# Optimization experiments

Hardware: AMD Instinct MI355X
Metric: run time of the kernel (lower is better)

## Reference

```python
import jax, jax.numpy as jnp
import numpy as np

N_HEAD = 16

def setup_inputs() -> dict:
    key = jax.random.key(0)
    ks = jax.random.split(key, 5)
    B, T, C = 4, 2048, 1024
    x = jax.random.normal(ks[0], (B, T, C), dtype=jnp.float32)
    # Linear params (torch nn.Linear: y = x @ W.T + b), init scaled like default
    s = 1.0 / np.sqrt(C)
    W_attn = jax.random.uniform(ks[1], (3 * C, C), dtype=jnp.float32, minval=-s, maxval=s)
    b_attn = jax.random.uniform(ks[2], (3 * C,), dtype=jnp.float32, minval=-s, maxval=s)
    W_proj = jax.random.uniform(ks[3], (C, C), dtype=jnp.float32, minval=-s, maxval=s)
    b_proj = jax.random.uniform(ks[4], (C,), dtype=jnp.float32, minval=-s, maxval=s)
    return {"x": x, "W_attn": W_attn, "b_attn": b_attn, "W_proj": W_proj, "b_proj": b_proj}

def reference(x, W_attn, b_attn, W_proj, b_proj):
    B, T, C = x.shape
    H = N_HEAD
    D = C // H
    qkv = jnp.einsum('btc,oc->bto', x, W_attn) + b_attn  # [B,T,3C]
    q, k, v = jnp.split(qkv, 3, axis=2)
    # [B,H,T,D]
    q = q.reshape(B, T, H, D).transpose(0, 2, 1, 3)
    k = k.reshape(B, T, H, D).transpose(0, 2, 1, 3)
    v = v.reshape(B, T, H, D).transpose(0, 2, 1, 3)
    att = jnp.einsum('bhtd,bhsd->bhts', q, k) * (1.0 / np.sqrt(D))  # [B,H,T,T]
    causal = jnp.tril(jnp.ones((T, T), dtype=bool))
    att = jnp.where(causal, att, -jnp.inf)
    att = jax.nn.softmax(att, axis=-1)
    y = jnp.einsum('bhts,bhsd->bhtd', att, v)  # [B,H,T,D]
    y = y.transpose(0, 2, 1, 3).reshape(B, T, C)
    return jnp.einsum('btc,oc->bto', y, W_proj) + b_proj
```

## Files before the change

### kernel.cpp

```cpp
#include <hip/hip_runtime.h>
#include <stdint.h>

typedef unsigned short u16;
typedef __attribute__((ext_vector_type(8))) short short8;
typedef __attribute__((ext_vector_type(4))) float float4v;

#define MFMA16(a, b, c) __builtin_amdgcn_mfma_f32_16x16x32_bf16((a), (b), (c), 0, 0, 0)

#define Q_SCALE 0.18033688011112042f

__device__ __forceinline__ int swz(int row, int col) {
  return row * 64 + (col & 7) + ((((col >> 3) ^ row) & 7) << 3);
}

__device__ __forceinline__ u16 f2b(float f) {
  union { float f; unsigned u; } x; x.f = f;
  unsigned r = x.u + 0x7fffu + ((x.u >> 16) & 1u);
  return (u16)(r >> 16);
}

__device__ __forceinline__ unsigned pack2(float a, float b) {
  return (unsigned)f2b(a) | ((unsigned)f2b(b) << 16);
}

__device__ __forceinline__ void load_lds_16(const void* g, void* l) {
  __builtin_amdgcn_global_load_lds((__attribute__((address_space(1))) void*)g,
                                   (__attribute__((address_space(3))) void*)l,
                                   16, 0, 0);
}

__global__ __launch_bounds__(256) void cvt_bf16(const float* __restrict__ in,
                                                u16* __restrict__ out, int n8) {
  int i = blockIdx.x * 256 + threadIdx.x;
  if (i >= n8) return;
  const float4* p = (const float4*)in + (size_t)i * 2;
  float4 a = p[0], b = p[1];
  uint4 w;
  w.x = pack2(a.x, a.y);
  w.y = pack2(a.z, a.w);
  w.z = pack2(b.x, b.y);
  w.w = pack2(b.z, b.w);
  *(uint4*)&out[(size_t)i * 8] = w;
}

__global__ __launch_bounds__(256) void transpose_v(const u16* __restrict__ V,
                                                   u16* __restrict__ Vt) {
  __shared__ u16 tile[64][72];
  const int bh = blockIdx.y;
  const int t0 = blockIdx.x * 64;
  const int tid = threadIdx.x;
  const int r = tid >> 3, c = (tid & 7) * 8;
#pragma unroll
  for (int h = 0; h < 2; ++h) {
    uint4 v = *(const uint4*)&V[((size_t)bh * 2048 + t0 + r + h * 32) * 64 + c];
    const u16* p = (const u16*)&v;
#pragma unroll
    for (int j = 0; j < 8; ++j) tile[c + j][r + h * 32] = p[j];
  }
  __syncthreads();
#pragma unroll
  for (int h = 0; h < 2; ++h) {
    uint4 w;
    u16* p = (u16*)&w;
#pragma unroll
    for (int j = 0; j < 8; ++j) p[j] = tile[r + h * 32][c + j];
    *(uint4*)&Vt[((size_t)bh * 64 + r + h * 32) * 2048 + t0 + c] = w;
  }
}

template <bool QKV_OUT>
__global__ __launch_bounds__(256) void gemm_bt(const u16* __restrict__ A,
                                               const u16* __restrict__ B,
                                               const float* __restrict__ bias,
                                               float* __restrict__ Cf,
                                               u16* __restrict__ QKV,
                                               int M, int N, int K) {
  __shared__ __align__(16) u16 As[128 * 64];
  __shared__ __align__(16) u16 Bs[128 * 64];
  const int tid = threadIdx.x;
  const int lane = tid & 63;
  const int wave = tid >> 6;
  const int quad = lane >> 4;
  const int l15 = lane & 15;
  const int bm0 = blockIdx.y * 128;
  const int bn0 = blockIdx.x * 128;
  const int wm = (wave & 1) * 64;
  const int wn = (wave >> 1) * 64;

  float4v acc[4][4];
#pragma unroll
  for (int i = 0; i < 4; ++i)
#pragma unroll
    for (int j = 0; j < 4; ++j) acc[i][j] = (float4v){0.f, 0.f, 0.f, 0.f};

  const int srow = wave * 32 + (lane >> 3);
  const int scol = ((lane & 7) ^ ((lane >> 3) & 7)) * 8;

  for (int k0 = 0; k0 < K; k0 += 64) {
#pragma unroll
    for (int s = 0; s < 4; ++s) {
      const int r = s * 8;
      load_lds_16(&A[(size_t)(bm0 + srow + r) * K + k0 + scol], &As[(wave * 32 + r) * 64]);
      load_lds_16(&B[(size_t)(bn0 + srow + r) * K + k0 + scol], &Bs[(wave * 32 + r) * 64]);
    }
    __builtin_amdgcn_s_waitcnt(0);
    __syncthreads();
#pragma unroll
    for (int ks = 0; ks < 2; ++ks) {
      short8 af[4], bf[4];
#pragma unroll
      for (int t = 0; t < 4; ++t) {
        af[t] = *(const short8*)&As[swz(wm + t * 16 + l15, ks * 32 + quad * 8)];
        bf[t] = *(const short8*)&Bs[swz(wn + t * 16 + l15, ks * 32 + quad * 8)];
      }
#pragma unroll
      for (int mt = 0; mt < 4; ++mt)
#pragma unroll
        for (int nt = 0; nt < 4; ++nt)
          acc[mt][nt] = MFMA16(af[mt], bf[nt], acc[mt][nt]);
    }
    __syncthreads();
  }

#pragma unroll
  for (int mt = 0; mt < 4; ++mt) {
    const int row0 = bm0 + wm + mt * 16 + quad * 4;
#pragma unroll
    for (int nt = 0; nt < 4; ++nt) {
      const int col = bn0 + wn + nt * 16 + l15;
      const float bs = bias[col];
      if constexpr (QKV_OUT) {
        const int which = col >> 10;
        const int rem = col & 1023;
        const int h = rem >> 6;
        const int d = rem & 63;
        const float sc = (which == 0) ? Q_SCALE : 1.0f;
#pragma unroll
        for (int i = 0; i < 4; ++i) {
          const int t = row0 + i;
          const int b = t >> 11;
          const int tt = t & 2047;
          QKV[(size_t)which * 8388608 +
              ((size_t)(b * 16 + h) * 2048 + tt) * 64 + d] = f2b((acc[mt][nt][i] + bs) * sc);
        }
      } else {
#pragma unroll
        for (int i = 0; i < 4; ++i)
          Cf[(size_t)(row0 + i) * N + col] = acc[mt][nt][i] + bs;
      }
    }
  }
}

__global__ __launch_bounds__(256) void attn_kernel(const u16* __restrict__ QKV,
                                                   const u16* __restrict__ Vt_g,
                                                   u16* __restrict__ Y) {
  const int bx = blockIdx.x;
  const int bh = blockIdx.y;
  const int b = bh >> 4, h = bh & 15;
  const int tid = threadIdx.x;
  const int lane = tid & 63;
  const int wave = tid >> 6;
  const int quad = lane >> 4;
  const int l15 = lane & 15;
  const int qt[2] = {bx, 31 - bx};

  const u16* Qg = QKV + (size_t)bh * 2048 * 64;
  const u16* Kg = QKV + 8388608 + (size_t)bh * 2048 * 64;
  const u16* Vg = Vt_g + (size_t)bh * 64 * 2048;

  __shared__ __align__(16) u16 Ks[2][64 * 64];
  __shared__ __align__(16) u16 Vt[2][64 * 64];

  short8 qf[2][2];
#pragma unroll
  for (int u = 0; u < 2; ++u)
#pragma unroll
    for (int ks = 0; ks < 2; ++ks)
      qf[u][ks] = *(const short8*)&Qg[(size_t)(qt[u] * 64 + wave * 16 + l15) * 64 + ks * 32 + quad * 8];

  float4v o[2][4];
  float rs[2] = {0.f, 0.f};
#pragma unroll
  for (int u = 0; u < 2; ++u)
#pragma unroll
    for (int i = 0; i < 4; ++i) o[u][i] = (float4v){0.f, 0.f, 0.f, 0.f};

  const int idxA = (l15 + ((quad & 1) << 5)) << 2;
  const int idxB = idxA + 64;

  const int r8 = lane >> 3;
  const int c8 = ((lane & 7) ^ r8) * 8;
  auto stage = [&](int st_, int bufi) {
    const int sb = st_ * 64;
#pragma unroll
    for (int p = 0; p < 2; ++p) {
      const int c = wave * 2 + p;
      load_lds_16(&Kg[(size_t)(sb + c * 8 + r8) * 64 + c8], &Ks[bufi][c * 512]);
      load_lds_16(&Vg[(size_t)(c * 8 + r8) * 2048 + sb + c8], &Vt[bufi][c * 512]);
    }
  };

  const int last = qt[1];
  stage(0, 0);
  __builtin_amdgcn_s_waitcnt(0);
  __syncthreads();

  for (int st = 0; st <= last; ++st) {
    const int cur = st & 1;
    if (st < last) stage(st + 1, cur ^ 1);
    const bool both = (st <= qt[0]);

    float4v s[2][4];
#pragma unroll
    for (int u = 0; u < 2; ++u)
#pragma unroll
      for (int nt = 0; nt < 4; ++nt) s[u][nt] = (float4v){0.f, 0.f, 0.f, 0.f};
    __builtin_amdgcn_s_setprio(1);
#pragma unroll
    for (int ks = 0; ks < 2; ++ks)
#pragma unroll
      for (int nt = 0; nt < 4; ++nt) {
        const short8 kf = *(const short8*)&Ks[cur][swz(nt * 16 + l15, ks * 32 + quad * 8)];
        s[1][nt] = MFMA16(kf, qf[1][ks], s[1][nt]);
        if (both) s[0][nt] = MFMA16(kf, qf[0][ks], s[0][nt]);
      }
    __builtin_amdgcn_s_setprio(0);

    short8 af[2][2];
    const bool hi = quad >= 2;
#pragma unroll
    for (int u = 0; u < 2; ++u) {
      if (u == 0 && !both) continue;

      if (st == qt[u]) {
        const int qrow = wave * 16 + l15;
        const int kb = quad * 4;
#pragma unroll
        for (int nt = 0; nt < 4; ++nt)
#pragma unroll
          for (int i = 0; i < 4; ++i)
            if (kb + nt * 16 + i > qrow) s[u][nt][i] = -1e30f;
      }

      uint2 pk[4];
#pragma unroll
      for (int nt = 0; nt < 4; ++nt) {
        const float p0 = __builtin_amdgcn_exp2f(s[u][nt][0]);
        const float p1 = __builtin_amdgcn_exp2f(s[u][nt][1]);
        const float p2 = __builtin_amdgcn_exp2f(s[u][nt][2]);
        const float p3 = __builtin_amdgcn_exp2f(s[u][nt][3]);
        rs[u] += (p0 + p1) + (p2 + p3);
        pk[nt].x = pack2(p0, p1);
        pk[nt].y = pack2(p2, p3);
      }

#pragma unroll
      for (int ks = 0; ks < 2; ++ks) {
        const int a0 = __builtin_amdgcn_ds_bpermute(idxA, (int)pk[2 * ks].x);
        const int a1 = __builtin_amdgcn_ds_bpermute(idxA, (int)pk[2 * ks].y);
        const int b0 = __builtin_amdgcn_ds_bpermute(idxA, (int)pk[2 * ks + 1].x);
        const int b1 = __builtin_amdgcn_ds_bpermute(idxA, (int)pk[2 * ks + 1].y);
        const int c0 = __builtin_amdgcn_ds_bpermute(idxB, (int)pk[2 * ks].x);
        const int c1 = __builtin_amdgcn_ds_bpermute(idxB, (int)pk[2 * ks].y);
        const int d0 = __builtin_amdgcn_ds_bpermute(idxB, (int)pk[2 * ks + 1].x);
        const int d1 = __builtin_amdgcn_ds_bpermute(idxB, (int)pk[2 * ks + 1].y);
        uint4 w;
        w.x = (unsigned)(hi ? b0 : a0);
        w.y = (unsigned)(hi ? b1 : a1);
        w.z = (unsigned)(hi ? d0 : c0);
        w.w = (unsigned)(hi ? d1 : c1);
        af[u][ks] = *(const short8*)&w;
      }
    }

    __builtin_amdgcn_s_setprio(1);
#pragma unroll
    for (int ks = 0; ks < 2; ++ks)
#pragma unroll
      for (int dt = 0; dt < 4; ++dt) {
        const short8 vf = *(const short8*)&Vt[cur][swz(dt * 16 + l15, ks * 32 + quad * 8)];
        o[1][dt] = MFMA16(af[1][ks], vf, o[1][dt]);
        if (both) o[0][dt] = MFMA16(af[0][ks], vf, o[0][dt]);
      }
    __builtin_amdgcn_s_setprio(0);

    __builtin_amdgcn_s_waitcnt(0);
    __syncthreads();
  }

#pragma unroll
  for (int u = 0; u < 2; ++u) {
    float r = rs[u];
    r += __shfl_xor(r, 16);
    r += __shfl_xor(r, 32);
    float linv[4];
#pragma unroll
    for (int i = 0; i < 4; ++i) linv[i] = 1.0f / __shfl(r, quad * 4 + i);
#pragma unroll
    for (int dt = 0; dt < 4; ++dt)
#pragma unroll
      for (int i = 0; i < 4; ++i) {
        const float v = o[u][dt][i] * linv[i];
        const int t = qt[u] * 64 + wave * 16 + quad * 4 + i;
        Y[((size_t)b * 2048 + t) * 1024 + h * 64 + dt * 16 + l15] = f2b(v);
      }
  }
}

extern "C" void kernel_launch(void* const* d_in, const int* in_sizes, int n_in,
                              void* d_out, int out_size, void* d_ws, size_t ws_size,
                              hipStream_t stream) {
  const float* x  = (const float*)d_in[0];
  const float* Wa = (const float*)d_in[1];
  const float* ba = (const float*)d_in[2];
  const float* Wp = (const float*)d_in[3];
  const float* bp = (const float*)d_in[4];
  float* out = (float*)d_out;

  u16* xb  = (u16*)d_ws;
  u16* Wab = xb + 8388608;
  u16* Wpb = Wab + 3145728;
  u16* qkv = Wpb + 1048576;
  u16* y   = xb;
  u16* vt  = (u16*)d_out;

  cvt_bf16<<<4096, 256, 0, stream>>>(x, xb, 1048576);
  cvt_bf16<<<1536, 256, 0, stream>>>(Wa, Wab, 393216);
  cvt_bf16<<<512, 256, 0, stream>>>(Wp, Wpb, 131072);

  gemm_bt<true><<<dim3(24, 64), 256, 0, stream>>>(xb, Wab, ba, nullptr, qkv, 8192, 3072, 1024);
  transpose_v<<<dim3(32, 64), 256, 0, stream>>>(qkv + 16777216, vt);
  attn_kernel<<<dim3(16, 64), 256, 0, stream>>>(qkv, vt, y);
  gemm_bt<false><<<dim3(8, 64), 256, 0, stream>>>(y, Wpb, bp, out, nullptr, 8192, 1024, 1024);
}
```

Baseline: 315.7 us.

## Triple-buffer K/V tiles with partial vmcnt waits and use permlane swaps

Moves K/V LDS staging from double to triple buffering. Tiles are prefetched two steps ahead, and each iteration waits only on the older loads (vmcnt(4)) instead of draining every outstanding load, so global latency overlaps more compute. It also replaces the eight ds_bpermute shuffles per k-slice, used to rearrange P into MFMA A-operand layout, with v_permlane32/16_swap register swaps that avoid LDS traffic. The costs are more LDS per block, which may lower occupancy, and a correctness dependence on the permlane swap pattern matching the old layout and on the vmcnt counts matching the number of issued loads.

```diff
diff --git a/kernel.cpp b/kernel.cpp
--- a/kernel.cpp
+++ b/kernel.cpp
@@ -169,8 +169,8 @@
   const u16* Kg = QKV + 8388608 + (size_t)bh * 2048 * 64;
   const u16* Vg = Vt_g + (size_t)bh * 64 * 2048;
 
-  __shared__ __align__(16) u16 Ks[2][64 * 64];
-  __shared__ __align__(16) u16 Vt[2][64 * 64];
+  __shared__ __align__(16) u16 Ks[3][64 * 64];
+  __shared__ __align__(16) u16 Vt[3][64 * 64];
 
   short8 qf[2][2];
 #pragma unroll
@@ -185,9 +185,6 @@
   for (int u = 0; u < 2; ++u)
 #pragma unroll
     for (int i = 0; i < 4; ++i) o[u][i] = (float4v){0.f, 0.f, 0.f, 0.f};
-
-  const int idxA = (l15 + ((quad & 1) << 5)) << 2;
-  const int idxB = idxA + 64;
 
   const int r8 = lane >> 3;
   const int c8 = ((lane & 7) ^ r8) * 8;
@@ -203,12 +200,17 @@
 
   const int last = qt[1];
   stage(0, 0);
-  __builtin_amdgcn_s_waitcnt(0);
-  __syncthreads();
-
+  stage(1, 1);
+  asm volatile("s_waitcnt vmcnt(4)" ::: "memory");
+  __builtin_amdgcn_s_barrier();
+
+  int cur = 0;
   for (int st = 0; st <= last; ++st) {
-    const int cur = st & 1;
-    if (st < last) stage(st + 1, cur ^ 1);
+    const bool pf = (st + 2 <= last);
+    if (pf) {
+      int nb = cur + 2; if (nb >= 3) nb -= 3;
+      stage(st + 2, nb);
+    }
     const bool both = (st <= qt[0]);
 
     float4v s[2][4];
@@ -228,7 +230,6 @@
     __builtin_amdgcn_s_setprio(0);
 
     short8 af[2][2];
-    const bool hi = quad >= 2;
 #pragma unroll
     for (int u = 0; u < 2; ++u) {
       if (u == 0 && !both) continue;
@@ -243,7 +244,7 @@
             if (kb + nt * 16 + i > qrow) s[u][nt][i] = -1e30f;
       }
 
-      uint2 pk[4];
+      unsigned pkx[4], pky[4];
 #pragma unroll
       for (int nt = 0; nt < 4; ++nt) {
         const float p0 = __builtin_amdgcn_exp2f(s[u][nt][0]);
@@ -251,25 +252,20 @@
         const float p2 = __builtin_amdgcn_exp2f(s[u][nt][2]);
         const float p3 = __builtin_amdgcn_exp2f(s[u][nt][3]);
         rs[u] += (p0 + p1) + (p2 + p3);
-        pk[nt].x = pack2(p0, p1);
-        pk[nt].y = pack2(p2, p3);
+        pkx[nt] = pack2(p0, p1);
+        pky[nt] = pack2(p2, p3);
       }
 
 #pragma unroll
       for (int ks = 0; ks < 2; ++ks) {
-        const int a0 = __builtin_amdgcn_ds_bpermute(idxA, (int)pk[2 * ks].x);
-        const int a1 = __builtin_amdgcn_ds_bpermute(idxA, (int)pk[2 * ks].y);
-        const int b0 = __builtin_amdgcn_ds_bpermute(idxA, (int)pk[2 * ks + 1].x);
-        const int b1 = __builtin_amdgcn_ds_bpermute(idxA, (int)pk[2 * ks + 1].y);
-        const int c0 = __builtin_amdgcn_ds_bpermute(idxB, (int)pk[2 * ks].x);
-        const int c1 = __builtin_amdgcn_ds_bpermute(idxB, (int)pk[2 * ks].y);
-        const int d0 = __builtin_amdgcn_ds_bpermute(idxB, (int)pk[2 * ks + 1].x);
-        const int d1 = __builtin_amdgcn_ds_bpermute(idxB, (int)pk[2 * ks + 1].y);
+        unsigned ax = pkx[2 * ks], bx2 = pkx[2 * ks + 1];
+        unsigned ay = pky[2 * ks], by2 = pky[2 * ks + 1];
+        asm("v_permlane32_swap_b32 %0, %1" : "+v"(ax), "+v"(bx2));
+        asm("v_permlane16_swap_b32 %0, %1" : "+v"(ax), "+v"(bx2));
+        asm("v_permlane32_swap_b32 %0, %1" : "+v"(ay), "+v"(by2));
+        asm("v_permlane16_swap_b32 %0, %1" : "+v"(ay), "+v"(by2));
         uint4 w;
-        w.x = (unsigned)(hi ? b0 : a0);
-        w.y = (unsigned)(hi ? b1 : a1);
-        w.z = (unsigned)(hi ? d0 : c0);
-        w.w = (unsigned)(hi ? d1 : c1);
+        w.x = ax; w.y = ay; w.z = bx2; w.w = by2;
         af[u][ks] = *(const short8*)&w;
       }
     }
@@ -285,8 +281,11 @@
       }
     __builtin_amdgcn_s_setprio(0);
 
-    __builtin_amdgcn_s_waitcnt(0);
-    __syncthreads();
+    if (pf) asm volatile("s_waitcnt vmcnt(4)" ::: "memory");
+    else    asm volatile("s_waitcnt vmcnt(0)" ::: "memory");
+    __builtin_amdgcn_s_barrier();
+
+    ++cur; if (cur >= 3) cur = 0;
   }
 
 #pragma unroll
```

Result: faster. 299.8 us (-5.0%).
